# Kernel optimization log

Measured on AMD Instinct MI355X. Metric: run time of the kernel, lower is better.

## Reference

```python
import jax, jax.numpy as jnp
import numpy as np

N, E = 4096, 4096          # nodes, hyperedges
IN_DIM, OUT_DIM, EDGE_DIM = 256, 256, 64
HEADS, DEG, CARD = 8, 8, 8  # node degree, edge cardinality (regular hypergraph)


def setup_inputs() -> dict:
    key = jax.random.key(0)
    ks = jax.random.split(key, 6)
    # regular hypergraph: DEG rounds, each a permutation of nodes chunked into
    # blocks of CARD -> every node in exactly DEG edges, every edge has CARD
    # distinct nodes. E = DEG * N / CARD.
    rng = np.random.default_rng(0)
    node_of_edge = np.concatenate(
        [rng.permutation(N).reshape(-1, CARD) for _ in range(DEG)], axis=0)  # [E, CARD]
    inc = np.zeros((E, N), dtype=np.float32)
    inc[np.arange(E)[:, None], node_of_edge] = 1.0
    s = 0.05
    return {
        "x": jax.random.normal(ks[0], (N, IN_DIM), jnp.float32),
        "incidence": jnp.asarray(inc),
        "edge_attr": jax.random.normal(ks[1], (E, EDGE_DIM), jnp.float32),
        "W_lin": jax.random.normal(ks[2], (IN_DIM, OUT_DIM), jnp.float32) * s,
        "W_edge": jax.random.normal(ks[3], (EDGE_DIM, OUT_DIM), jnp.float32) * s,
        "in_proj_w": jax.random.normal(ks[4], (3 * OUT_DIM, OUT_DIM), jnp.float32) * s,
        "in_proj_b": jnp.zeros((3 * OUT_DIM,), jnp.float32),
        "out_proj_w": jax.random.normal(ks[5], (OUT_DIM, OUT_DIM), jnp.float32) * s,
        "out_proj_b": jnp.zeros((OUT_DIM,), jnp.float32),
        "deg": DEG,
        "card": CARD,
    }


def reference(x, incidence, edge_attr, W_lin, W_edge,
              in_proj_w, in_proj_b, out_proj_w, out_proj_b, deg, card):
    n = x.shape[0]
    Wh = x @ W_lin          # [N, D]
    We = edge_attr @ W_edge  # [E, D]
    Dm = Wh.shape[1]
    H = HEADS
    dh = Dm // H
    # recover regular structure from the binary incidence matrix.
    # (attention is permutation-invariant over the pair set, so the order of
    #  indices returned by top_k vs torch.nonzero does not matter)
    _, edge_of_node = jax.lax.top_k(incidence.T, deg)   # [N, deg]
    _, node_of_edge = jax.lax.top_k(incidence, card)    # [E, card]
    pair_e = edge_of_node[:, :, None]                   # [N, deg, 1]
    pair_u = node_of_edge[edge_of_node]                 # [N, deg, card]
    L = deg * card
    Ksrc = (Wh[pair_u] + We[pair_e]).reshape(n, L, Dm)  # key source per pair
    Vsrc = Wh[pair_u].reshape(n, L, Dm)                 # value source per pair
    # torch nn.MultiheadAttention in/out projections
    Wq, Wk, Wv = jnp.split(in_proj_w, 3, axis=0)
    bq, bk, bv = jnp.split(in_proj_b, 3)
    q = (Wh @ Wq.T + bq).reshape(n, H, dh)              # q_len = 1 per node
    k = (Ksrc @ Wk.T + bk).reshape(n, L, H, dh)
    v = (Vsrc @ Wv.T + bv).reshape(n, L, H, dh)
    scale = 1.0 / jnp.sqrt(jnp.asarray(dh, q.dtype))
    scores = jnp.einsum('nhd,nlhd->nhl', q, k) * scale  # [N, H, L]
    attn = jax.nn.softmax(scores, axis=-1)
    ctx = jnp.einsum('nhl,nlhd->nhd', attn, v).reshape(n, Dm)
    out = ctx @ out_proj_w.T + out_proj_b
    return jax.nn.relu(out)
```

## Files before the change

kernel.cpp:

```cpp
#include <hip/hip_runtime.h>
#include <hip/hip_bf16.h>

#define NN    4096
#define EE    4096
#define DM    256
#define EDIM  64
#define HH    8
#define DHd   32
#define LL    64

typedef short  s16x8 __attribute__((ext_vector_type(8)));
typedef unsigned short u16x8 __attribute__((ext_vector_type(8)));
typedef float  f32x4 __attribute__((ext_vector_type(4)));

__device__ __forceinline__ float b2f(unsigned short u) {
  return __uint_as_float(((unsigned int)u) << 16);
}
__device__ __forceinline__ unsigned short f2b_bits(float f) {
  unsigned int u = __float_as_uint(f);
  u = (u + 0x7FFFu + ((u >> 16) & 1u)) >> 16;
  return (unsigned short)u;
}

__global__ __launch_bounds__(256) void f2b_all(
    const float* __restrict__ x, const float* __restrict__ ea,
    const float* __restrict__ ipw, const float* __restrict__ wlin,
    const float* __restrict__ wedge, const float* __restrict__ wout,
    unsigned short* __restrict__ xb, unsigned short* __restrict__ eab,
    unsigned short* __restrict__ ipwb, unsigned short* __restrict__ wlinb,
    unsigned short* __restrict__ wedgeb, unsigned short* __restrict__ woutb,
    int* __restrict__ cnt) {
  int i = blockIdx.x * 256 + threadIdx.x;
  if (i < 8192) cnt[i] = 0;
  const float* src; unsigned short* dst; int j = i;
  if (j < 262144)       { src = x;     dst = xb; }
  else { j -= 262144;
  if (j < 65536)        { src = ea;    dst = eab; }
  else { j -= 65536;
  if (j < 49152)        { src = ipw;   dst = ipwb; }
  else { j -= 49152;
  if (j < 16384)        { src = wlin;  dst = wlinb; }
  else { j -= 16384;
  if (j < 4096)         { src = wedge; dst = wedgeb; }
  else { j -= 4096;
  if (j >= 16384) return;
                          src = wout;  dst = woutb; }}}}}
  float4 v = ((const float4*)src)[j];
  ushort4 o;
  o.x = f2b_bits(v.x); o.y = f2b_bits(v.y); o.z = f2b_bits(v.z); o.w = f2b_bits(v.w);
  ((ushort4*)dst)[j] = o;
}

__global__ __launch_bounds__(256) void build_adj(const float* __restrict__ inc,
                                                 int* __restrict__ cnt_e,
                                                 int* __restrict__ cnt_n,
                                                 int* __restrict__ noe,
                                                 int* __restrict__ eon) {
  int t = blockIdx.x * 256 + threadIdx.x;
  float4 v = ((const float4*)inc)[t];
  int flat = t * 4;
  int e  = flat >> 12;
  int u0 = flat & 4095;
  float vals[4] = {v.x, v.y, v.z, v.w};
#pragma unroll
  for (int j = 0; j < 4; ++j) {
    if (vals[j] != 0.0f) {
      int u  = u0 + j;
      int pe = atomicAdd(&cnt_e[e], 1);
      noe[e * 8 + pe] = u;
      int pn = atomicAdd(&cnt_n[u], 1);
      eon[u * 8 + pn] = e;
    }
  }
}

#define MODE_PLAIN 0
#define MODE_PROJ  1
#define MODE_OUT   2

__global__ __launch_bounds__(256) void gemm_bt(
    const unsigned short* __restrict__ A, const unsigned short* __restrict__ B,
    int M, int N, int K, int mode,
    float* __restrict__ out_f, unsigned short* __restrict__ out_b,
    unsigned short* __restrict__ out_b2, const float* __restrict__ bias) {
  __shared__ short As[64 * 40] __attribute__((aligned(16)));
  __shared__ short Bs[64 * 40] __attribute__((aligned(16)));
  const int tid  = threadIdx.x;
  const int wid  = tid >> 6, lane = tid & 63;
  const int i0   = blockIdx.x * 64, j0 = blockIdx.y * 64;
  const int wr   = (wid >> 1) * 32, wc = (wid & 1) * 32;
  const int srow = tid >> 2, schunk = (tid & 3) * 8;
  const int fr   = lane & 15, fk = (lane >> 4) * 8;

  f32x4 acc[2][2];
#pragma unroll
  for (int a = 0; a < 2; ++a)
#pragma unroll
    for (int b = 0; b < 2; ++b) acc[a][b] = (f32x4){0.f, 0.f, 0.f, 0.f};

  for (int kk = 0; kk < K; kk += 32) {
    *(s16x8*)&As[srow * 40 + schunk] = *(const s16x8*)&A[(size_t)(i0 + srow) * K + kk + schunk];
    *(s16x8*)&Bs[srow * 40 + schunk] = *(const s16x8*)&B[(size_t)(j0 + srow) * K + kk + schunk];
    __syncthreads();
    s16x8 af0 = *(const s16x8*)&As[(wr + fr) * 40 + fk];
    s16x8 af1 = *(const s16x8*)&As[(wr + 16 + fr) * 40 + fk];
    s16x8 bf0 = *(const s16x8*)&Bs[(wc + fr) * 40 + fk];
    s16x8 bf1 = *(const s16x8*)&Bs[(wc + 16 + fr) * 40 + fk];
    acc[0][0] = __builtin_amdgcn_mfma_f32_16x16x32_bf16(af0, bf0, acc[0][0], 0, 0, 0);
    acc[0][1] = __builtin_amdgcn_mfma_f32_16x16x32_bf16(af0, bf1, acc[0][1], 0, 0, 0);
    acc[1][0] = __builtin_amdgcn_mfma_f32_16x16x32_bf16(af1, bf0, acc[1][0], 0, 0, 0);
    acc[1][1] = __builtin_amdgcn_mfma_f32_16x16x32_bf16(af1, bf1, acc[1][1], 0, 0, 0);
    __syncthreads();
  }

  const int ecol = lane & 15, erow0 = (lane >> 4) * 4;
#pragma unroll
  for (int mi = 0; mi < 2; ++mi)
#pragma unroll
    for (int ni = 0; ni < 2; ++ni) {
#pragma unroll
      for (int v = 0; v < 4; ++v) {
        int i = i0 + wr + mi * 16 + erow0 + v;
        int j = j0 + wc + ni * 16 + ecol;
        float val = acc[mi][ni][v];
        if (mode == MODE_PLAIN) {
          out_b[(size_t)i * N + j] = f2b_bits(val);
        } else if (mode == MODE_PROJ) {
          if (j < 256)      out_f[(size_t)i * 256 + j]          = val + bias[j];
          else if (j < 512) out_b[(size_t)i * 256 + (j - 256)]  = f2b_bits(val);
          else              out_b2[(size_t)i * 256 + (j - 512)] = f2b_bits(val + bias[j]);
        } else {
          float r = val + bias[j];
          out_f[(size_t)i * N + j] = r > 0.f ? r : 0.f;
        }
      }
    }
}

__global__ __launch_bounds__(256) void fuse_w(
    const unsigned short* __restrict__ ipw, const unsigned short* __restrict__ wlin,
    const unsigned short* __restrict__ wedge,
    unsigned short* __restrict__ F, unsigned short* __restrict__ G) {
  const int gpart = (blockIdx.y == 4);
  if (gpart && blockIdx.x >= 4) return;
  const unsigned short* A = gpart ? (ipw + (size_t)(256 + blockIdx.x * 64) * 256)
                                  : (ipw + (size_t)blockIdx.x * 64 * 256);
  const unsigned short* B = gpart ? wedge : wlin;
  unsigned short* outp = gpart ? G : F;
  const int j0 = gpart ? 0 : blockIdx.y * 64;
  const int outN = gpart ? 64 : 256;
  const int i0 = blockIdx.x * 64;

  __shared__ short As[64 * 40] __attribute__((aligned(16)));
  __shared__ short Bs[64 * 40] __attribute__((aligned(16)));
  const int tid  = threadIdx.x;
  const int wid  = tid >> 6, lane = tid & 63;
  const int wr   = (wid >> 1) * 32, wc = (wid & 1) * 32;
  const int srow = tid >> 2, schunk = (tid & 3) * 8;
  const int fr   = lane & 15, fk = (lane >> 4) * 8;

  f32x4 acc[2][2];
#pragma unroll
  for (int a = 0; a < 2; ++a)
#pragma unroll
    for (int b = 0; b < 2; ++b) acc[a][b] = (f32x4){0.f, 0.f, 0.f, 0.f};

  for (int kk = 0; kk < 256; kk += 32) {
    *(s16x8*)&As[srow * 40 + schunk] = *(const s16x8*)&A[(size_t)srow * 256 + kk + schunk];
    *(s16x8*)&Bs[srow * 40 + schunk] = *(const s16x8*)&B[(size_t)(j0 + srow) * 256 + kk + schunk];
    __syncthreads();
    s16x8 af0 = *(const s16x8*)&As[(wr + fr) * 40 + fk];
    s16x8 af1 = *(const s16x8*)&As[(wr + 16 + fr) * 40 + fk];
    s16x8 bf0 = *(const s16x8*)&Bs[(wc + fr) * 40 + fk];
    s16x8 bf1 = *(const s16x8*)&Bs[(wc + 16 + fr) * 40 + fk];
    acc[0][0] = __builtin_amdgcn_mfma_f32_16x16x32_bf16(af0, bf0, acc[0][0], 0, 0, 0);
    acc[0][1] = __builtin_amdgcn_mfma_f32_16x16x32_bf16(af0, bf1, acc[0][1], 0, 0, 0);
    acc[1][0] = __builtin_amdgcn_mfma_f32_16x16x32_bf16(af1, bf0, acc[1][0], 0, 0, 0);
    acc[1][1] = __builtin_amdgcn_mfma_f32_16x16x32_bf16(af1, bf1, acc[1][1], 0, 0, 0);
    __syncthreads();
  }

  const int ecol = lane & 15, erow0 = (lane >> 4) * 4;
#pragma unroll
  for (int mi = 0; mi < 2; ++mi)
#pragma unroll
    for (int ni = 0; ni < 2; ++ni)
#pragma unroll
      for (int v = 0; v < 4; ++v) {
        int i = i0 + wr + mi * 16 + erow0 + v;
        int j = j0 + wc + ni * 16 + ecol;
        if (j < outN) outp[(size_t)i * outN + j] = f2b_bits(acc[mi][ni][v]);
      }
}

__global__ __launch_bounds__(512) void attn_kernel(
    const float* __restrict__ q, const unsigned short* __restrict__ Kn,
    const unsigned short* __restrict__ Vn, const unsigned short* __restrict__ Ke,
    const int* __restrict__ eon, const int* __restrict__ noe,
    unsigned short* __restrict__ ctx) {
  const int n = blockIdx.x;
  __shared__ int   e_s[8];
  __shared__ int   u_s[64];
  __shared__ float q_s[256];
  __shared__ float qke_s[64];
  __shared__ float attn_s[8][64];
  __shared__ unsigned short Vg[64 * 256] __attribute__((aligned(16)));
  const int tid = threadIdx.x;
  if (tid < 8) e_s[tid] = eon[n * 8 + tid];
  if (tid >= 256) q_s[tid - 256] = q[(size_t)n * 256 + (tid - 256)];
  __syncthreads();
  if (tid < 64) {
    u_s[tid] = noe[e_s[tid >> 3] * 8 + (tid & 7)];
  } else if (tid < 128) {
    const int h = (tid - 64) >> 3, e = tid & 7;
    const u16x8* ep = (const u16x8*)(Ke + (size_t)e_s[e] * 256 + h * 32);
    float s = 0.f;
#pragma unroll
    for (int c = 0; c < 4; ++c) {
      u16x8 ev = ep[c];
#pragma unroll
      for (int j = 0; j < 8; ++j) s += q_s[h * 32 + c * 8 + j] * b2f(ev[j]);
    }
    qke_s[(h << 3) | e] = s;
  }
  __syncthreads();

  u16x8 vstage[4];
  int vrow[4];
#pragma unroll
  for (int i = 0; i < 4; ++i) {
    int chunk = i * 512 + tid;
    vrow[i] = chunk >> 5;
    int col = (chunk & 31) * 8;
    vstage[i] = *(const u16x8*)(Vn + (size_t)u_s[vrow[i]] * 256 + col);
  }

  const int h = tid >> 6, l = tid & 63;
  const int u = u_s[l];
  const u16x8* kp = (const u16x8*)(Kn + ((size_t)u * 256 + h * 32));
  float s = 0.f;
#pragma unroll
  for (int c = 0; c < 4; ++c) {
    u16x8 kv = kp[c];
#pragma unroll
    for (int j = 0; j < 8; ++j) s += q_s[h * 32 + c * 8 + j] * b2f(kv[j]);
  }
  s = (s + qke_s[(h << 3) | (l >> 3)]) * 0.17677669529663687f;

  float m = s;
#pragma unroll
  for (int off = 32; off >= 1; off >>= 1) m = fmaxf(m, __shfl_xor(m, off));
  float p = __expf(s - m);
  float sum = p;
#pragma unroll
  for (int off = 32; off >= 1; off >>= 1) sum += __shfl_xor(sum, off);
  attn_s[h][l] = p / sum;

#pragma unroll
  for (int i = 0; i < 4; ++i) {
    int chunk = i * 512 + tid;
    *(u16x8*)&Vg[(size_t)chunk * 8] = vstage[i];
  }
  __syncthreads();

  const int d = l & 31, half = l >> 5;
  const unsigned short* vp = &Vg[(size_t)(half * 32) * 256 + h * 32 + d];
  const float* ap = &attn_s[h][half * 32];
  float acc = 0.f;
#pragma unroll
  for (int t2 = 0; t2 < 32; ++t2)
    acc += ap[t2] * b2f(vp[t2 * 256]);
  acc += __shfl_xor(acc, 32);
  if (half == 0) ctx[(size_t)n * 256 + h * 32 + d] = f2b_bits(acc);
}

#define OFF_Q      ((size_t)0)
#define OFF_KN     ((size_t)4194304)
#define OFF_VN     ((size_t)6291456)
#define OFF_KE     ((size_t)8388608)
#define OFF_CTX    ((size_t)10485760)
#define OFF_XBF    ((size_t)12582912)
#define OFF_EABF   ((size_t)14680064)
#define OFF_WOUTBF ((size_t)15204352)
#define OFF_IPWBF  ((size_t)15335424)
#define OFF_WLINBF ((size_t)15728640)
#define OFF_WEDGBF ((size_t)15859712)
#define OFF_F      ((size_t)15892480)
#define OFF_G      ((size_t)16285696)
#define OFF_CNTE   ((size_t)16318464)
#define OFF_CNTN   ((size_t)16334848)
#define OFF_NOE    ((size_t)16351232)
#define OFF_EON    ((size_t)16482304)

extern "C" void kernel_launch(void* const* d_in, const int* in_sizes, int n_in,
                              void* d_out, int out_size, void* d_ws, size_t ws_size,
                              hipStream_t stream) {
  const float* x     = (const float*)d_in[0];
  const float* inc   = (const float*)d_in[1];
  const float* ea    = (const float*)d_in[2];
  const float* wlin  = (const float*)d_in[3];
  const float* wedge = (const float*)d_in[4];
  const float* ipw   = (const float*)d_in[5];
  const float* ipb   = (const float*)d_in[6];
  const float* wout  = (const float*)d_in[7];
  const float* outb  = (const float*)d_in[8];

  char* ws = (char*)d_ws;
  float*          q       = (float*)(ws + OFF_Q);
  unsigned short* Kn      = (unsigned short*)(ws + OFF_KN);
  unsigned short* Vn      = (unsigned short*)(ws + OFF_VN);
  unsigned short* Ke      = (unsigned short*)(ws + OFF_KE);
  unsigned short* ctx     = (unsigned short*)(ws + OFF_CTX);
  unsigned short* x_bf    = (unsigned short*)(ws + OFF_XBF);
  unsigned short* ea_bf   = (unsigned short*)(ws + OFF_EABF);
  unsigned short* wout_bf = (unsigned short*)(ws + OFF_WOUTBF);
  unsigned short* ipw_bf  = (unsigned short*)(ws + OFF_IPWBF);
  unsigned short* wlin_bf = (unsigned short*)(ws + OFF_WLINBF);
  unsigned short* wedg_bf = (unsigned short*)(ws + OFF_WEDGBF);
  unsigned short* F       = (unsigned short*)(ws + OFF_F);
  unsigned short* G       = (unsigned short*)(ws + OFF_G);
  int*            cnt_e   = (int*)(ws + OFF_CNTE);
  int*            cnt_n   = (int*)(ws + OFF_CNTN);
  int*            noe     = (int*)(ws + OFF_NOE);
  int*            eon     = (int*)(ws + OFF_EON);

  f2b_all<<<1616, 256, 0, stream>>>(x, ea, ipw, wlin, wedge, wout,
                                    x_bf, ea_bf, ipw_bf, wlin_bf, wedg_bf, wout_bf,
                                    cnt_e);
  build_adj<<<16384, 256, 0, stream>>>(inc, cnt_e, cnt_n, noe, eon);
  fuse_w<<<dim3(12, 5), 256, 0, stream>>>(ipw_bf, wlin_bf, wedg_bf, F, G);
  gemm_bt<<<dim3(64, 12), 256, 0, stream>>>(x_bf, F, 4096, 768, 256,
                                            MODE_PROJ, q, Kn, Vn, ipb);
  gemm_bt<<<dim3(64, 4), 256, 0, stream>>>(ea_bf, G, 4096, 256, 64,
                                           MODE_PLAIN, nullptr, Ke, nullptr, nullptr);
  attn_kernel<<<4096, 512, 0, stream>>>(q, Kn, Vn, Ke, eon, noe, ctx);
  gemm_bt<<<dim3(64, 4), 256, 0, stream>>>(ctx, wout_bf, 4096, 256, 256,
                                           MODE_OUT, (float*)d_out, nullptr, nullptr, outb);
}
```

Measured before the change: 88.67 us.

## Merge independent launches and compute attention context from registers via shuffles

Puts the adjacency build and the weight-fusion GEMM into one launch, and the Q/K/V projection and edge-key GEMMs into another, so the pipeline needs fewer kernel launches and the small GEMMs no longer sit idle in their own launches. The attention kernel drops its 32KB shared V tile and its attention-weight buffer. Each lane now loads its own V fragments and accumulates context with wave shuffles, which removes a barrier and cuts LDS use so more blocks can be resident. The cost is more shuffle reduction work per wave, and the smaller tile blocks now share a launch with the very large adjacency grid.

Result: faster. 83.51 us (-5.8%).

```diff
diff --git a/kernel.cpp b/kernel.cpp
--- a/kernel.cpp
+++ b/kernel.cpp
@@ -51,43 +51,18 @@
   ((ushort4*)dst)[j] = o;
 }
 
-__global__ __launch_bounds__(256) void build_adj(const float* __restrict__ inc,
-                                                 int* __restrict__ cnt_e,
-                                                 int* __restrict__ cnt_n,
-                                                 int* __restrict__ noe,
-                                                 int* __restrict__ eon) {
-  int t = blockIdx.x * 256 + threadIdx.x;
-  float4 v = ((const float4*)inc)[t];
-  int flat = t * 4;
-  int e  = flat >> 12;
-  int u0 = flat & 4095;
-  float vals[4] = {v.x, v.y, v.z, v.w};
-#pragma unroll
-  for (int j = 0; j < 4; ++j) {
-    if (vals[j] != 0.0f) {
-      int u  = u0 + j;
-      int pe = atomicAdd(&cnt_e[e], 1);
-      noe[e * 8 + pe] = u;
-      int pn = atomicAdd(&cnt_n[u], 1);
-      eon[u * 8 + pn] = e;
-    }
-  }
-}
-
 #define MODE_PLAIN 0
 #define MODE_PROJ  1
 #define MODE_OUT   2
 
-__global__ __launch_bounds__(256) void gemm_bt(
+__device__ __forceinline__ void gemm_tile(
     const unsigned short* __restrict__ A, const unsigned short* __restrict__ B,
-    int M, int N, int K, int mode,
+    int i0, int j0, int N, int K, int mode,
     float* __restrict__ out_f, unsigned short* __restrict__ out_b,
-    unsigned short* __restrict__ out_b2, const float* __restrict__ bias) {
-  __shared__ short As[64 * 40] __attribute__((aligned(16)));
-  __shared__ short Bs[64 * 40] __attribute__((aligned(16)));
+    unsigned short* __restrict__ out_b2, const float* __restrict__ bias,
+    short* As, short* Bs) {
   const int tid  = threadIdx.x;
   const int wid  = tid >> 6, lane = tid & 63;
-  const int i0   = blockIdx.x * 64, j0 = blockIdx.y * 64;
   const int wr   = (wid >> 1) * 32, wc = (wid & 1) * 32;
   const int srow = tid >> 2, schunk = (tid & 3) * 8;
   const int fr   = lane & 15, fk = (lane >> 4) * 8;
@@ -137,60 +112,70 @@
     }
 }
 
-__global__ __launch_bounds__(256) void fuse_w(
-    const unsigned short* __restrict__ ipw, const unsigned short* __restrict__ wlin,
-    const unsigned short* __restrict__ wedge,
+__global__ __launch_bounds__(256) void adj_fusew(
+    const float* __restrict__ inc,
+    int* __restrict__ cnt_e, int* __restrict__ cnt_n,
+    int* __restrict__ noe, int* __restrict__ eon,
+    const unsigned short* __restrict__ ipw_bf, const unsigned short* __restrict__ wlin_bf,
+    const unsigned short* __restrict__ wedg_bf,
     unsigned short* __restrict__ F, unsigned short* __restrict__ G) {
-  const int gpart = (blockIdx.y == 4);
-  if (gpart && blockIdx.x >= 4) return;
-  const unsigned short* A = gpart ? (ipw + (size_t)(256 + blockIdx.x * 64) * 256)
-                                  : (ipw + (size_t)blockIdx.x * 64 * 256);
-  const unsigned short* B = gpart ? wedge : wlin;
-  unsigned short* outp = gpart ? G : F;
-  const int j0 = gpart ? 0 : blockIdx.y * 64;
-  const int outN = gpart ? 64 : 256;
-  const int i0 = blockIdx.x * 64;
-
   __shared__ short As[64 * 40] __attribute__((aligned(16)));
   __shared__ short Bs[64 * 40] __attribute__((aligned(16)));
-  const int tid  = threadIdx.x;
-  const int wid  = tid >> 6, lane = tid & 63;
-  const int wr   = (wid >> 1) * 32, wc = (wid & 1) * 32;
-  const int srow = tid >> 2, schunk = (tid & 3) * 8;
-  const int fr   = lane & 15, fk = (lane >> 4) * 8;
-
-  f32x4 acc[2][2];
-#pragma unroll
-  for (int a = 0; a < 2; ++a)
-#pragma unroll
-    for (int b = 0; b < 2; ++b) acc[a][b] = (f32x4){0.f, 0.f, 0.f, 0.f};
-
-  for (int kk = 0; kk < 256; kk += 32) {
-    *(s16x8*)&As[srow * 40 + schunk] = *(const s16x8*)&A[(size_t)srow * 256 + kk + schunk];
-    *(s16x8*)&Bs[srow * 40 + schunk] = *(const s16x8*)&B[(size_t)(j0 + srow) * 256 + kk + schunk];
-    __syncthreads();
-    s16x8 af0 = *(const s16x8*)&As[(wr + fr) * 40 + fk];
-    s16x8 af1 = *(const s16x8*)&As[(wr + 16 + fr) * 40 + fk];
-    s16x8 bf0 = *(const s16x8*)&Bs[(wc + fr) * 40 + fk];
-    s16x8 bf1 = *(const s16x8*)&Bs[(wc + 16 + fr) * 40 + fk];
-    acc[0][0] = __builtin_amdgcn_mfma_f32_16x16x32_bf16(af0, bf0, acc[0][0], 0, 0, 0);
-    acc[0][1] = __builtin_amdgcn_mfma_f32_16x16x32_bf16(af0, bf1, acc[0][1], 0, 0, 0);
-    acc[1][0] = __builtin_amdgcn_mfma_f32_16x16x32_bf16(af1, bf0, acc[1][0], 0, 0, 0);
-    acc[1][1] = __builtin_amdgcn_mfma_f32_16x16x32_bf16(af1, bf1, acc[1][1], 0, 0, 0);
-    __syncthreads();
-  }
-
-  const int ecol = lane & 15, erow0 = (lane >> 4) * 4;
-#pragma unroll
-  for (int mi = 0; mi < 2; ++mi)
-#pragma unroll
-    for (int ni = 0; ni < 2; ++ni)
-#pragma unroll
-      for (int v = 0; v < 4; ++v) {
-        int i = i0 + wr + mi * 16 + erow0 + v;
-        int j = j0 + wc + ni * 16 + ecol;
-        if (j < outN) outp[(size_t)i * outN + j] = f2b_bits(acc[mi][ni][v]);
+  const int bid = blockIdx.x;
+  if (bid < 16384) {
+    int t = bid * 256 + threadIdx.x;
+    float4 v = ((const float4*)inc)[t];
+    int flat = t * 4;
+    int e  = flat >> 12;
+    int u0 = flat & 4095;
+    float vals[4] = {v.x, v.y, v.z, v.w};
+#pragma unroll
+    for (int j = 0; j < 4; ++j) {
+      if (vals[j] != 0.0f) {
+        int u  = u0 + j;
+        int pe = atomicAdd(&cnt_e[e], 1);
+        noe[e * 8 + pe] = u;
+        int pn = atomicAdd(&cnt_n[u], 1);
+        eon[u * 8 + pn] = e;
       }
+    }
+    return;
+  }
+  int fb = bid - 16384;
+  if (fb < 48) {
+    gemm_tile(ipw_bf, wlin_bf, (fb >> 2) * 64, (fb & 3) * 64, 256, 256,
+              MODE_PLAIN, nullptr, F, nullptr, nullptr, As, Bs);
+  } else {
+    gemm_tile(ipw_bf + 256 * 256, wedg_bf, (fb - 48) * 64, 0, 64, 256,
+              MODE_PLAIN, nullptr, G, nullptr, nullptr, As, Bs);
+  }
+}
+
+__global__ __launch_bounds__(256) void proj_ke(
+    const unsigned short* __restrict__ x_bf, const unsigned short* __restrict__ F,
+    const unsigned short* __restrict__ ea_bf, const unsigned short* __restrict__ G,
+    float* __restrict__ q, unsigned short* __restrict__ Kn, unsigned short* __restrict__ Vn,
+    unsigned short* __restrict__ Ke, const float* __restrict__ ipb) {
+  __shared__ short As[64 * 40] __attribute__((aligned(16)));
+  __shared__ short Bs[64 * 40] __attribute__((aligned(16)));
+  const int bid = blockIdx.x;
+  if (bid < 768) {
+    gemm_tile(x_bf, F, (bid & 63) * 64, (bid >> 6) * 64, 768, 256,
+              MODE_PROJ, q, Kn, Vn, ipb, As, Bs);
+  } else {
+    int r = bid - 768;
+    gemm_tile(ea_bf, G, (r & 63) * 64, (r >> 6) * 64, 256, 64,
+              MODE_PLAIN, nullptr, Ke, nullptr, nullptr, As, Bs);
+  }
+}
+
+__global__ __launch_bounds__(256) void gemm_out(
+    const unsigned short* __restrict__ ctx, const unsigned short* __restrict__ wout_bf,
+    float* __restrict__ out, const float* __restrict__ bias) {
+  __shared__ short As[64 * 40] __attribute__((aligned(16)));
+  __shared__ short Bs[64 * 40] __attribute__((aligned(16)));
+  gemm_tile(ctx, wout_bf, blockIdx.x * 64, blockIdx.y * 64, 256, 256,
+            MODE_OUT, out, nullptr, nullptr, bias, As, Bs);
 }
 
 __global__ __launch_bounds__(512) void attn_kernel(
@@ -203,11 +188,10 @@
   __shared__ int   u_s[64];
   __shared__ float q_s[256];
   __shared__ float qke_s[64];
-  __shared__ float attn_s[8][64];
-  __shared__ unsigned short Vg[64 * 256] __attribute__((aligned(16)));
   const int tid = threadIdx.x;
   if (tid < 8) e_s[tid] = eon[n * 8 + tid];
-  if (tid >= 256) q_s[tid - 256] = q[(size_t)n * 256 + (tid - 256)];
+  if (tid >= 256 && tid < 320)
+    ((float4*)q_s)[tid - 256] = ((const float4*)(q + (size_t)n * 256))[tid - 256];
   __syncthreads();
   if (tid < 64) {
     u_s[tid] = noe[e_s[tid >> 3] * 8 + (tid & 7)];
@@ -225,18 +209,15 @@
   }
   __syncthreads();
 
+  const int h = tid >> 6, lane = tid & 63;
+  const int dchunk = lane >> 4, rg = lane & 15;
+
   u16x8 vstage[4];
-  int vrow[4];
-#pragma unroll
-  for (int i = 0; i < 4; ++i) {
-    int chunk = i * 512 + tid;
-    vrow[i] = chunk >> 5;
-    int col = (chunk & 31) * 8;
-    vstage[i] = *(const u16x8*)(Vn + (size_t)u_s[vrow[i]] * 256 + col);
-  }
-
-  const int h = tid >> 6, l = tid & 63;
-  const int u = u_s[l];
+#pragma unroll
+  for (int i = 0; i < 4; ++i)
+    vstage[i] = *(const u16x8*)(Vn + (size_t)u_s[rg * 4 + i] * 256 + h * 32 + dchunk * 8);
+
+  const int u = u_s[lane];
   const u16x8* kp = (const u16x8*)(Kn + ((size_t)u * 256 + h * 32));
   float s = 0.f;
 #pragma unroll
@@ -245,7 +226,7 @@
 #pragma unroll
     for (int j = 0; j < 8; ++j) s += q_s[h * 32 + c * 8 + j] * b2f(kv[j]);
   }
-  s = (s + qke_s[(h << 3) | (l >> 3)]) * 0.17677669529663687f;
+  s = (s + qke_s[(h << 3) | (lane >> 3)]) * 0.17677669529663687f;
 
   float m = s;
 #pragma unroll
@@ -254,24 +235,28 @@
   float sum = p;
 #pragma unroll
   for (int off = 32; off >= 1; off >>= 1) sum += __shfl_xor(sum, off);
-  attn_s[h][l] = p / sum;
-
+  const float a = p / sum;
+
+  float acc[8];
+#pragma unroll
+  for (int j = 0; j < 8; ++j) acc[j] = 0.f;
 #pragma unroll
   for (int i = 0; i < 4; ++i) {
-    int chunk = i * 512 + tid;
-    *(u16x8*)&Vg[(size_t)chunk * 8] = vstage[i];
-  }
-  __syncthreads();
-
-  const int d = l & 31, half = l >> 5;
-  const unsigned short* vp = &Vg[(size_t)(half * 32) * 256 + h * 32 + d];
-  const float* ap = &attn_s[h][half * 32];
-  float acc = 0.f;
-#pragma unroll
-  for (int t2 = 0; t2 < 32; ++t2)
-    acc += ap[t2] * b2f(vp[t2 * 256]);
-  acc += __shfl_xor(acc, 32);
-  if (half == 0) ctx[(size_t)n * 256 + h * 32 + d] = f2b_bits(acc);
+    float pi = __shfl(a, rg * 4 + i, 64);
+#pragma unroll
+    for (int j = 0; j < 8; ++j) acc[j] += pi * b2f(vstage[i][j]);
+  }
+#pragma unroll
+  for (int off = 1; off < 16; off <<= 1)
+#pragma unroll
+    for (int j = 0; j < 8; ++j) acc[j] += __shfl_xor(acc[j], off, 64);
+
+  if (rg == 0) {
+    u16x8 o;
+#pragma unroll
+    for (int j = 0; j < 8; ++j) o[j] = f2b_bits(acc[j]);
+    *(u16x8*)(ctx + (size_t)n * 256 + h * 32 + dchunk * 8) = o;
+  }
 }
 
 #define OFF_Q      ((size_t)0)
@@ -327,13 +312,9 @@
   f2b_all<<<1616, 256, 0, stream>>>(x, ea, ipw, wlin, wedge, wout,
                                     x_bf, ea_bf, ipw_bf, wlin_bf, wedg_bf, wout_bf,
                                     cnt_e);
-  build_adj<<<16384, 256, 0, stream>>>(inc, cnt_e, cnt_n, noe, eon);
-  fuse_w<<<dim3(12, 5), 256, 0, stream>>>(ipw_bf, wlin_bf, wedg_bf, F, G);
-  gemm_bt<<<dim3(64, 12), 256, 0, stream>>>(x_bf, F, 4096, 768, 256,
-                                            MODE_PROJ, q, Kn, Vn, ipb);
-  gemm_bt<<<dim3(64, 4), 256, 0, stream>>>(ea_bf, G, 4096, 256, 64,
-                                           MODE_PLAIN, nullptr, Ke, nullptr, nullptr);
+  adj_fusew<<<16436, 256, 0, stream>>>(inc, cnt_e, cnt_n, noe, eon,
+                                       ipw_bf, wlin_bf, wedg_bf, F, G);
+  proj_ke<<<1024, 256, 0, stream>>>(x_bf, F, ea_bf, G, q, Kn, Vn, Ke, ipb);
   attn_kernel<<<4096, 512, 0, stream>>>(q, Kn, Vn, Ke, eon, noe, ctx);
-  gemm_bt<<<dim3(64, 4), 256, 0, stream>>>(ctx, wout_bf, 4096, 256, 256,
-                                           MODE_OUT, (float*)d_out, nullptr, nullptr, outb);
-}
+  gemm_out<<<dim3(64, 4), 256, 0, stream>>>(ctx, wout_bf, (float*)d_out, outb);
+}
```
